# Kernel optimization log

Measured on AMD Instinct MI355X. Metric: run time of the kernel, lower is better.

The kernel has to match this reference:

```python
import jax, jax.numpy as jnp
import numpy as np

C = 64
G = 4
K = 3
GC = C // G
OS = 1.0  # offset_scale
OM_DIM = int(np.ceil(G * K * K * 3 / 8) * 8)  # 112, padded; only first G*27 used


def setup_inputs() -> dict:
    key = jax.random.key(0)
    ks = jax.random.split(key, 8)
    B, H, W = 2, 384, 384
    s = 0.02
    return {
        "inp": jax.random.normal(ks[0], (B, C, H, W), jnp.float32),
        "Wv": jax.random.normal(ks[1], (C, C), jnp.float32) * s,
        "bv": jnp.zeros((C,), jnp.float32),
        "Wdw": jax.random.normal(ks[2], (C, 1, K, K), jnp.float32) * s,
        "bdw": jnp.zeros((C,), jnp.float32),
        "Wom": jax.random.normal(ks[3], (C, OM_DIM), jnp.float32) * s,
        "bom": jnp.zeros((OM_DIM,), jnp.float32),
        "Wo": jax.random.normal(ks[4], (C, C), jnp.float32) * s,
    }


def _bilinear(v, px, py, H, W, b_idx, g_idx):
    # v: (B,H,W,G,GC); px,py: (B,H,W,G) pixel coords; zero padding outside.
    x0 = jnp.floor(px)
    y0 = jnp.floor(py)
    wx1 = px - x0
    wy1 = py - y0
    x0i = x0.astype(jnp.int32)
    y0i = y0.astype(jnp.int32)
    out = jnp.zeros(px.shape + (v.shape[-1],), v.dtype)
    for dy, wy in ((0, 1.0 - wy1), (1, wy1)):
        for dx, wx in ((0, 1.0 - wx1), (1, wx1)):
            xi = x0i + dx
            yi = y0i + dy
            valid = ((xi >= 0) & (xi < W) & (yi >= 0) & (yi < H)).astype(v.dtype)
            xc = jnp.clip(xi, 0, W - 1)
            yc = jnp.clip(yi, 0, H - 1)
            g = v[b_idx, yc, xc, g_idx]  # (B,H,W,G,GC)
            out = out + g * (wy * wx * valid)[..., None]
    return out


def reference(inp, Wv, bv, Wdw, bdw, Wom, bom, Wo):
    B, _, H, W = inp.shape
    x = inp.transpose(0, 2, 3, 1)  # (B,H,W,C)
    # value projection, split into groups
    value = (x @ Wv + bv).reshape(B, H, W, G, GC)
    # depthwise conv on input feeds the offset/mask predictor
    dw = jax.lax.conv_general_dilated(
        inp, Wdw, window_strides=(1, 1), padding=[(1, 1), (1, 1)],
        feature_group_count=C) + bdw[None, :, None, None]
    om = dw.transpose(0, 2, 3, 1) @ Wom + bom  # (B,H,W,OM_DIM)
    om = om[..., : G * K * K * 3].reshape(B, H, W, G, K * K * 3)
    off = om[..., : K * K * 2].reshape(B, H, W, G, K * K, 2)  # (dx,dy) per point
    mask = om[..., K * K * 2:]  # (B,H,W,G,K*K), no softmax in DCNv4

    base_x = jnp.arange(W, dtype=value.dtype)[None, None, :, None]
    base_y = jnp.arange(H, dtype=value.dtype)[None, :, None, None]
    b_idx = jnp.arange(B)[:, None, None, None]
    g_idx = jnp.arange(G)[None, None, None, :]

    out = jnp.zeros((B, H, W, G, GC), value.dtype)
    k = 0
    for ky in range(K):
        for kx in range(K):
            dx = off[..., k, 0]
            dy = off[..., k, 1]
            px = base_x + ((kx - K // 2) + dx) * OS
            py = base_y + ((ky - K // 2) + dy) * OS
            samp = _bilinear(value, px, py, H, W, b_idx, g_idx)
            out = out + samp * mask[..., k][..., None]
            k += 1

    out = out.reshape(B, H, W, C) @ Wo  # output_proj, no bias (output_bias=False)
    return out.transpose(0, 3, 1, 2)  # back to (B,C,H,W)
```

## Files before the change

kernel.cpp:

```cpp
#include <hip/hip_runtime.h>
#include <hip/hip_fp16.h>
#include <math.h>

namespace {
constexpr int kH = 384, kW = 384, kBn = 2;
constexpr int kHW = kH * kW;
constexpr int kOMD = 112;
constexpr int kNB = kBn * (kHW / 64);
constexpr int kNB8 = kNB / 8;
}

typedef _Float16 h2 __attribute__((ext_vector_type(2)));
typedef _Float16 half8 __attribute__((ext_vector_type(8)));
typedef float f32x4 __attribute__((ext_vector_type(4)));

__device__ unsigned g_Wom2[32 * kOMD];
__device__ unsigned g_Wo2[32 * 64];
__device__ __align__(16) _Float16 g_WvFh[4 * 2 * 64 * 8];
__device__ __align__(16) _Float16 g_WvFl[4 * 2 * 64 * 8];

__device__ __forceinline__ int swz(int t) {
    return (t & 7) * kNB8 + (t >> 3);
}

__device__ __forceinline__ unsigned pack2h(float a, float b) {
    unsigned short lo = __builtin_bit_cast(unsigned short, __float2half_rn(a));
    unsigned short hi = __builtin_bit_cast(unsigned short, __float2half_rn(b));
    return (unsigned)lo | ((unsigned)hi << 16);
}

#if __has_builtin(__builtin_amdgcn_fdot2)
__device__ __forceinline__ float dot2(unsigned a, unsigned b, float c) {
    return __builtin_amdgcn_fdot2(__builtin_bit_cast(h2, a),
                                  __builtin_bit_cast(h2, b), c, false);
}
#else
__device__ __forceinline__ float dot2(unsigned a, unsigned b, float c) {
    h2 ha = __builtin_bit_cast(h2, a), hb = __builtin_bit_cast(h2, b);
    c = fmaf((float)ha.x, (float)hb.x, c);
    c = fmaf((float)ha.y, (float)hb.y, c);
    return c;
}
#endif

__device__ __forceinline__ void acc8h(__half2* pa, const unsigned short* src,
                                      float wgt) {
    const uint4 u0 = ((const uint4*)src)[0];
    const uint4 u1 = ((const uint4*)src)[1];
    const __half2 w2 = __half2half2(__float2half_rn(wgt));
    pa[0] = __hfma2(w2, __builtin_bit_cast(__half2, u0.x), pa[0]);
    pa[1] = __hfma2(w2, __builtin_bit_cast(__half2, u0.y), pa[1]);
    pa[2] = __hfma2(w2, __builtin_bit_cast(__half2, u0.z), pa[2]);
    pa[3] = __hfma2(w2, __builtin_bit_cast(__half2, u0.w), pa[3]);
    pa[4] = __hfma2(w2, __builtin_bit_cast(__half2, u1.x), pa[4]);
    pa[5] = __hfma2(w2, __builtin_bit_cast(__half2, u1.y), pa[5]);
    pa[6] = __hfma2(w2, __builtin_bit_cast(__half2, u1.z), pa[6]);
    pa[7] = __hfma2(w2, __builtin_bit_cast(__half2, u1.w), pa[7]);
}

__device__ __forceinline__ half8 ld_frag_g(const _Float16* ptr) {
    return __builtin_bit_cast(half8, *(const uint4*)ptr);
}

__global__ __launch_bounds__(256) void k_prep(
        const float* __restrict__ Wv, const float* __restrict__ Wom,
        const float* __restrict__ Wo) {
    const int gt = blockIdx.x * 256 + threadIdx.x;
    const int gstep = 64 * 256;
    for (int i = gt; i < 4 * 2 * 64 * 8; i += gstep) {
        const int jj = i & 7, l = (i >> 3) & 63, kh = (i >> 9) & 1, mt = i >> 10;
        const int co = mt * 16 + (l & 15);
        const int ch = kh * 32 + ((l >> 4) & 3) * 8 + jj;
        const float w = Wv[ch * 64 + co];
        const _Float16 hi = (_Float16)w;
        g_WvFh[i] = hi;
        g_WvFl[i] = (_Float16)((w - (float)hi) * 2048.f);
    }
    for (int i = gt; i < 32 * kOMD; i += gstep) {
        const int ci2 = i / kOMD, j = i % kOMD;
        g_Wom2[i] = pack2h(Wom[(2 * ci2) * kOMD + j],
                           Wom[(2 * ci2 + 1) * kOMD + j]);
    }
    for (int i = gt; i < 32 * 64; i += gstep) {
        const int ci2 = i >> 6, j = i & 63;
        g_Wo2[i] = pack2h(Wo[(2 * ci2) * 64 + j],
                          Wo[(2 * ci2 + 1) * 64 + j]);
    }
}

__global__ __launch_bounds__(256) void k_value(
        const float* __restrict__ inp, const float* __restrict__ bv,
        unsigned short* __restrict__ value) {
    const int tid = threadIdx.x;
    const int bid = swz(blockIdx.x);
    const int b = bid / (kHW / 64);
    const int pix0 = (bid % (kHW / 64)) * 64;
    const int l = tid & 63;
    const int wv = tid >> 6;
    const int lr = l & 15, q = l >> 4;
    const int gpx = pix0 + wv * 16 + lr;

    const float* xb = inp + (size_t)b * 64 * kHW + (size_t)(q * 8) * kHW + gpx;
    half8 bhf[2], blf[2];
    #pragma unroll
    for (int kh = 0; kh < 2; ++kh) {
        float xv[8];
        #pragma unroll
        for (int jj = 0; jj < 8; ++jj)
            xv[jj] = xb[(size_t)(kh * 32 + jj) * kHW];
        half8 hh, ll;
        #pragma unroll
        for (int jj = 0; jj < 8; ++jj) {
            const _Float16 hval = (_Float16)xv[jj];
            hh[jj] = hval;
            ll[jj] = (_Float16)((xv[jj] - (float)hval) * 2048.f);
        }
        bhf[kh] = hh;
        blf[kh] = ll;
    }

    #pragma unroll
    for (int mt = 0; mt < 4; ++mt) {
        const half8 ah0 = ld_frag_g(g_WvFh + ((mt * 2 + 0) * 64 + l) * 8);
        const half8 ah1 = ld_frag_g(g_WvFh + ((mt * 2 + 1) * 64 + l) * 8);
        const half8 al0 = ld_frag_g(g_WvFl + ((mt * 2 + 0) * 64 + l) * 8);
        const half8 al1 = ld_frag_g(g_WvFl + ((mt * 2 + 1) * 64 + l) * 8);
        f32x4 acc = {0.f, 0.f, 0.f, 0.f};
        f32x4 acc2 = {0.f, 0.f, 0.f, 0.f};
        acc  = __builtin_amdgcn_mfma_f32_16x16x32_f16(ah0, bhf[0], acc, 0, 0, 0);
        acc  = __builtin_amdgcn_mfma_f32_16x16x32_f16(ah1, bhf[1], acc, 0, 0, 0);
        acc2 = __builtin_amdgcn_mfma_f32_16x16x32_f16(ah0, blf[0], acc2, 0, 0, 0);
        acc2 = __builtin_amdgcn_mfma_f32_16x16x32_f16(ah1, blf[1], acc2, 0, 0, 0);
        acc2 = __builtin_amdgcn_mfma_f32_16x16x32_f16(al0, bhf[0], acc2, 0, 0, 0);
        acc2 = __builtin_amdgcn_mfma_f32_16x16x32_f16(al1, bhf[1], acc2, 0, 0, 0);
        const float4 b4 = *(const float4*)(bv + mt * 16 + q * 4);
        const float v0 = acc[0] + acc2[0] * (1.f / 2048.f) + b4.x;
        const float v1 = acc[1] + acc2[1] * (1.f / 2048.f) + b4.y;
        const float v2 = acc[2] + acc2[2] * (1.f / 2048.f) + b4.z;
        const float v3 = acc[3] + acc2[3] * (1.f / 2048.f) + b4.w;
        uint2 st;
        st.x = pack2h(v0, v1);
        st.y = pack2h(v2, v3);
        *(uint2*)(value + ((size_t)(b * 4 + mt) * kHW + gpx) * 16 + q * 4) = st;
    }
}

__global__ __launch_bounds__(256) void k_main(
        const float* __restrict__ inp, const float* __restrict__ Wdw,
        const float* __restrict__ bdw, const float* __restrict__ bom,
        const unsigned short* __restrict__ value, float* __restrict__ out) {
    __shared__ unsigned lds2[32][64];

    const int tid = threadIdx.x;
    const int bid = swz(blockIdx.x);
    const int b = bid / (kH * (kW / 64));
    const int rem = bid % (kH * (kW / 64));
    const int h = rem / (kW / 64);
    const int w0 = (rem % (kW / 64)) * 64;

    const int p = tid & 63;
    const int gs = __builtin_amdgcn_readfirstlane(tid >> 6);

    if (w0 != 0 && w0 != kW - 64) {
        const int i2 = p & 31;
        const int ch8 = p >> 5;
        const int xg = w0 + 2 * i2;
        float s0[8], s1[8];
        #pragma unroll 4
        for (int cc = 0; cc < 8; ++cc) {
            const int cA = gs * 16 + cc;
            const int cB = cA + 8;
            const float bsv = ch8 ? bdw[cB] : bdw[cA];
            float a0 = bsv, a1 = bsv;
            const float* ibA = inp + (size_t)(b * 64 + cA) * kHW;
            const float* wkA = Wdw + cA * 9;
            const float* wkB = Wdw + cB * 9;
            #pragma unroll
            for (int r = 0; r < 3; ++r) {
                const int y = h - 1 + r;
                if (y >= 0 && y < kH) {
                    const float* rowp = ibA + (size_t)(ch8 * 8) * kHW
                                            + (size_t)y * kW;
                    const float2 fc = *(const float2*)(rowp + xg);
                    const float xl = rowp[xg - 1];
                    const float xr = rowp[xg + 2];
                    const float k0 = ch8 ? wkB[r * 3 + 0] : wkA[r * 3 + 0];
                    const float k1 = ch8 ? wkB[r * 3 + 1] : wkA[r * 3 + 1];
                    const float k2 = ch8 ? wkB[r * 3 + 2] : wkA[r * 3 + 2];
                    a0 = fmaf(xl,   k0, a0);
                    a0 = fmaf(fc.x, k1, a0);
                    a0 = fmaf(fc.y, k2, a0);
                    a1 = fmaf(fc.x, k0, a1);
                    a1 = fmaf(fc.y, k1, a1);
                    a1 = fmaf(xr,   k2, a1);
                }
            }
            s0[cc] = a0;
            s1[cc] = a1;
        }
        #pragma unroll
        for (int e = 0; e < 4; ++e) {
            const int row = gs * 8 + ch8 * 4 + e;
            lds2[row][2 * i2]     = pack2h(s0[2 * e], s0[2 * e + 1]);
            lds2[row][2 * i2 + 1] = pack2h(s1[2 * e], s1[2 * e + 1]);
        }
    } else {
        const int w = w0 + p;
        #pragma unroll 2
        for (int q = 0; q < 8; ++q) {
            float sv[2];
            #pragma unroll
            for (int e = 0; e < 2; ++e) {
                const int c = gs * 16 + 2 * q + e;
                const float* ib = inp + (size_t)(b * 64 + c) * kHW;
                float s = bdw[c];
                #pragma unroll
                for (int r = 0; r < 3; ++r) {
                    const int y = h - 1 + r;
                    if (y >= 0 && y < kH) {
                        const float* rowp = ib + (size_t)y * kW;
                        #pragma unroll
                        for (int kx = 0; kx < 3; ++kx) {
                            const int x = w - 1 + kx;
                            const float v = (x >= 0 && x < kW) ? rowp[x] : 0.f;
                            s = fmaf(v, Wdw[c * 9 + r * 3 + kx], s);
                        }
                    }
                }
                sv[e] = s;
            }
            lds2[gs * 8 + q][p] = pack2h(sv[0], sv[1]);
        }
    }
    __syncthreads();

    float om[27];
    {
        const float* bg = bom + gs * 27;
        #pragma unroll
        for (int j = 0; j < 27; ++j) om[j] = bg[j];
        #pragma unroll 4
        for (int ci2 = 0; ci2 < 32; ++ci2) {
            const unsigned a2 = lds2[ci2][p];
            const unsigned* wr = g_Wom2 + ci2 * kOMD + gs * 27;
            #pragma unroll
            for (int j = 0; j < 27; ++j) om[j] = dot2(a2, wr[j], om[j]);
        }
    }
    __syncthreads();

    {
        __half2 pa[8];
        #pragma unroll
        for (int j = 0; j < 8; ++j) pa[j] = __builtin_bit_cast(__half2, 0u);
        const float fw = (float)(w0 + p);
        const float fh = (float)h;
        const unsigned short* vbase = value + (size_t)(b * 4 + gs) * kHW * 16;
        #pragma unroll
        for (int k = 0; k < 9; ++k) {
            const int ky = k / 3, kx = k % 3;
            const float dx = om[2 * k];
            const float dy = om[2 * k + 1];
            const float m = om[18 + k];
            const float px = fw + (float)(kx - 1) + dx;
            const float py = fh + (float)(ky - 1) + dy;
            const float x0f = floorf(px), y0f = floorf(py);
            const int x0 = (int)x0f, y0 = (int)y0f;
            const float wx1 = px - x0f, wy1 = py - y0f;
            const float wx0 = 1.f - wx1, wy0 = 1.f - wy1;
            const bool interior = (x0 >= 0) & (y0 >= 0) &
                                  (x0 < kW - 1) & (y0 < kH - 1);
            if (__all(interior)) {
                const unsigned short* b00 = vbase + ((size_t)y0 * kW + x0) * 16;
                const float wy0m = wy0 * m, wy1m = wy1 * m;
                acc8h(pa, b00,                wx0 * wy0m);
                acc8h(pa, b00 + 16,           wx1 * wy0m);
                acc8h(pa, b00 + kW * 16,      wx0 * wy1m);
                acc8h(pa, b00 + kW * 16 + 16, wx1 * wy1m);
            } else {
                #pragma unroll
                for (int cor = 0; cor < 4; ++cor) {
                    const int dy2 = cor >> 1, dx2 = cor & 1;
                    const int xi = x0 + dx2, yi = y0 + dy2;
                    float wgt = (dy2 ? wy1 : wy0) * (dx2 ? wx1 : wx0) * m;
                    if (xi < 0 || xi >= kW || yi < 0 || yi >= kH) wgt = 0.f;
                    const int xc = min(max(xi, 0), kW - 1);
                    const int yc = min(max(yi, 0), kH - 1);
                    acc8h(pa, vbase + ((size_t)yc * kW + xc) * 16, wgt);
                }
            }
        }
        #pragma unroll
        for (int j = 0; j < 8; ++j)
            lds2[gs * 8 + j][p] = __builtin_bit_cast(unsigned, pa[j]);
    }
    __syncthreads();

    {
        float acc[16];
        #pragma unroll
        for (int j = 0; j < 16; ++j) acc[j] = 0.f;
        #pragma unroll 4
        for (int ci2 = 0; ci2 < 32; ++ci2) {
            const unsigned a2 = lds2[ci2][p];
            const unsigned* wr = g_Wo2 + ci2 * 64 + gs * 16;
            #pragma unroll
            for (int j = 0; j < 16; ++j) acc[j] = dot2(a2, wr[j], acc[j]);
        }
        float* ob = out + (size_t)(b * 64 + gs * 16) * kHW + (size_t)h * kW + w0 + p;
        #pragma unroll
        for (int j = 0; j < 16; ++j) ob[(size_t)j * kHW] = acc[j];
    }
}

extern "C" void kernel_launch(void* const* d_in, const int* in_sizes, int n_in,
                              void* d_out, int out_size, void* d_ws, size_t ws_size,
                              hipStream_t stream) {
    const float* inp = (const float*)d_in[0];
    const float* Wv  = (const float*)d_in[1];
    const float* bv  = (const float*)d_in[2];
    const float* Wdw = (const float*)d_in[3];
    const float* bdw = (const float*)d_in[4];
    const float* Wom = (const float*)d_in[5];
    const float* bom = (const float*)d_in[6];
    const float* Wo  = (const float*)d_in[7];
    float* outp = (float*)d_out;
    unsigned short* value = (unsigned short*)d_ws;

    k_prep<<<64, 256, 0, stream>>>(Wv, Wom, Wo);
    k_value<<<kNB, 256, 0, stream>>>(inp, bv, value);
    k_main<<<kNB, 256, 0, stream>>>(inp, Wdw, bdw, bom, value, outp);
}
```

Baseline: 299.1 us.

## Split offset/mask prediction into a kernel co-scheduled with value projection

Interleaves value-projection blocks with depthwise-conv plus offset/mask blocks in a single launch, writing the offsets and masks as fp16 to a workspace buffer. A separate kernel then reads them and does the deformable sampling and output projection. The aim is to overlap the conv/offset compute with the memory-bound value projection and to lighten the sampling kernel, at the cost of extra global traffic and fp16 rounding of offsets. The previous two-kernel path is kept as a fallback when the workspace is too small.

```diff
diff --git a/kernel.cpp b/kernel.cpp
--- a/kernel.cpp
+++ b/kernel.cpp
@@ -8,6 +8,8 @@
 constexpr int kOMD = 112;
 constexpr int kNB = kBn * (kHW / 64);
 constexpr int kNB8 = kNB / 8;
+constexpr size_t kValBytes = (size_t)kBn * 4 * kHW * 16 * 2;
+constexpr size_t kOmBytes  = (size_t)kBn * 4 * kHW * 32 * 2;
 }
 
 typedef _Float16 h2 __attribute__((ext_vector_type(2)));
@@ -27,6 +29,15 @@
     unsigned short lo = __builtin_bit_cast(unsigned short, __float2half_rn(a));
     unsigned short hi = __builtin_bit_cast(unsigned short, __float2half_rn(b));
     return (unsigned)lo | ((unsigned)hi << 16);
+}
+
+__device__ __forceinline__ float h2f_lo(unsigned u) {
+    __half2 h = __builtin_bit_cast(__half2, u);
+    return __half2float(h.x);
+}
+__device__ __forceinline__ float h2f_hi(unsigned u) {
+    __half2 h = __builtin_bit_cast(__half2, u);
+    return __half2float(h.y);
 }
 
 #if __has_builtin(__builtin_amdgcn_fdot2)
@@ -62,43 +73,16 @@
     return __builtin_bit_cast(half8, *(const uint4*)ptr);
 }
 
-__global__ __launch_bounds__(256) void k_prep(
-        const float* __restrict__ Wv, const float* __restrict__ Wom,
-        const float* __restrict__ Wo) {
-    const int gt = blockIdx.x * 256 + threadIdx.x;
-    const int gstep = 64 * 256;
-    for (int i = gt; i < 4 * 2 * 64 * 8; i += gstep) {
-        const int jj = i & 7, l = (i >> 3) & 63, kh = (i >> 9) & 1, mt = i >> 10;
-        const int co = mt * 16 + (l & 15);
-        const int ch = kh * 32 + ((l >> 4) & 3) * 8 + jj;
-        const float w = Wv[ch * 64 + co];
-        const _Float16 hi = (_Float16)w;
-        g_WvFh[i] = hi;
-        g_WvFl[i] = (_Float16)((w - (float)hi) * 2048.f);
-    }
-    for (int i = gt; i < 32 * kOMD; i += gstep) {
-        const int ci2 = i / kOMD, j = i % kOMD;
-        g_Wom2[i] = pack2h(Wom[(2 * ci2) * kOMD + j],
-                           Wom[(2 * ci2 + 1) * kOMD + j]);
-    }
-    for (int i = gt; i < 32 * 64; i += gstep) {
-        const int ci2 = i >> 6, j = i & 63;
-        g_Wo2[i] = pack2h(Wo[(2 * ci2) * 64 + j],
-                          Wo[(2 * ci2 + 1) * 64 + j]);
-    }
-}
-
-__global__ __launch_bounds__(256) void k_value(
+
+__device__ __forceinline__ void value_body(
         const float* __restrict__ inp, const float* __restrict__ bv,
-        unsigned short* __restrict__ value) {
-    const int tid = threadIdx.x;
-    const int bid = swz(blockIdx.x);
+        unsigned short* __restrict__ value, int t, int tid) {
+    const int bid = swz(t);
     const int b = bid / (kHW / 64);
     const int pix0 = (bid % (kHW / 64)) * 64;
     const int l = tid & 63;
-    const int wv = tid >> 6;
-    const int lr = l & 15, q = l >> 4;
-    const int gpx = pix0 + wv * 16 + lr;
+    const int q = l >> 4;
+    const int gpx = pix0 + (tid >> 6) * 16 + (l & 15);
 
     const float* xb = inp + (size_t)b * 64 * kHW + (size_t)(q * 8) * kHW + gpx;
     half8 bhf[2], blf[2];
@@ -118,7 +102,6 @@
         bhf[kh] = hh;
         blf[kh] = ll;
     }
-
     #pragma unroll
     for (int mt = 0; mt < 4; ++mt) {
         const half8 ah0 = ld_frag_g(g_WvFh + ((mt * 2 + 0) * 64 + l) * 8);
@@ -134,33 +117,19 @@
         acc2 = __builtin_amdgcn_mfma_f32_16x16x32_f16(al0, bhf[0], acc2, 0, 0, 0);
         acc2 = __builtin_amdgcn_mfma_f32_16x16x32_f16(al1, bhf[1], acc2, 0, 0, 0);
         const float4 b4 = *(const float4*)(bv + mt * 16 + q * 4);
-        const float v0 = acc[0] + acc2[0] * (1.f / 2048.f) + b4.x;
-        const float v1 = acc[1] + acc2[1] * (1.f / 2048.f) + b4.y;
-        const float v2 = acc[2] + acc2[2] * (1.f / 2048.f) + b4.z;
-        const float v3 = acc[3] + acc2[3] * (1.f / 2048.f) + b4.w;
         uint2 st;
-        st.x = pack2h(v0, v1);
-        st.y = pack2h(v2, v3);
+        st.x = pack2h(acc[0] + acc2[0] * (1.f / 2048.f) + b4.x,
+                      acc[1] + acc2[1] * (1.f / 2048.f) + b4.y);
+        st.y = pack2h(acc[2] + acc2[2] * (1.f / 2048.f) + b4.z,
+                      acc[3] + acc2[3] * (1.f / 2048.f) + b4.w);
         *(uint2*)(value + ((size_t)(b * 4 + mt) * kHW + gpx) * 16 + q * 4) = st;
     }
 }
 
-__global__ __launch_bounds__(256) void k_main(
+__device__ __forceinline__ void stageA_conv(
         const float* __restrict__ inp, const float* __restrict__ Wdw,
-        const float* __restrict__ bdw, const float* __restrict__ bom,
-        const unsigned short* __restrict__ value, float* __restrict__ out) {
-    __shared__ unsigned lds2[32][64];
-
-    const int tid = threadIdx.x;
-    const int bid = swz(blockIdx.x);
-    const int b = bid / (kH * (kW / 64));
-    const int rem = bid % (kH * (kW / 64));
-    const int h = rem / (kW / 64);
-    const int w0 = (rem % (kW / 64)) * 64;
-
-    const int p = tid & 63;
-    const int gs = __builtin_amdgcn_readfirstlane(tid >> 6);
-
+        const float* __restrict__ bdw, int b, int h, int w0, int p, int gs,
+        unsigned (*lds2)[64]) {
     if (w0 != 0 && w0 != kW - 64) {
         const int i2 = p & 31;
         const int ch8 = p >> 5;
@@ -232,23 +201,27 @@
             lds2[gs * 8 + q][p] = pack2h(sv[0], sv[1]);
         }
     }
-    __syncthreads();
-
-    float om[27];
-    {
-        const float* bg = bom + gs * 27;
-        #pragma unroll
-        for (int j = 0; j < 27; ++j) om[j] = bg[j];
-        #pragma unroll 4
-        for (int ci2 = 0; ci2 < 32; ++ci2) {
-            const unsigned a2 = lds2[ci2][p];
-            const unsigned* wr = g_Wom2 + ci2 * kOMD + gs * 27;
-            #pragma unroll
-            for (int j = 0; j < 27; ++j) om[j] = dot2(a2, wr[j], om[j]);
-        }
-    }
-    __syncthreads();
-
+}
+
+__device__ __forceinline__ void stageB_om(
+        const float* __restrict__ bom, int p, int gs,
+        const unsigned (*lds2)[64], float* om) {
+    const float* bg = bom + gs * 27;
+    #pragma unroll
+    for (int j = 0; j < 27; ++j) om[j] = bg[j];
+    #pragma unroll 4
+    for (int ci2 = 0; ci2 < 32; ++ci2) {
+        const unsigned a2 = lds2[ci2][p];
+        const unsigned* wr = g_Wom2 + ci2 * kOMD + gs * 27;
+        #pragma unroll
+        for (int j = 0; j < 27; ++j) om[j] = dot2(a2, wr[j], om[j]);
+    }
+}
+
+__device__ __forceinline__ void stageCD(
+        const float* om, const unsigned short* __restrict__ value,
+        float* __restrict__ out, int b, int h, int w0, int p, int gs,
+        unsigned (*lds2)[64]) {
     {
         __half2 pa[8];
         #pragma unroll
@@ -295,7 +268,6 @@
             lds2[gs * 8 + j][p] = __builtin_bit_cast(unsigned, pa[j]);
     }
     __syncthreads();
-
     {
         float acc[16];
         #pragma unroll
@@ -311,6 +283,125 @@
         #pragma unroll
         for (int j = 0; j < 16; ++j) ob[(size_t)j * kHW] = acc[j];
     }
+}
+
+
+__global__ __launch_bounds__(256) void k_prep(
+        const float* __restrict__ Wv, const float* __restrict__ Wom,
+        const float* __restrict__ Wo) {
+    const int gt = blockIdx.x * 256 + threadIdx.x;
+    const int gstep = 64 * 256;
+    for (int i = gt; i < 4 * 2 * 64 * 8; i += gstep) {
+        const int jj = i & 7, l = (i >> 3) & 63, kh = (i >> 9) & 1, mt = i >> 10;
+        const int co = mt * 16 + (l & 15);
+        const int ch = kh * 32 + ((l >> 4) & 3) * 8 + jj;
+        const float w = Wv[ch * 64 + co];
+        const _Float16 hi = (_Float16)w;
+        g_WvFh[i] = hi;
+        g_WvFl[i] = (_Float16)((w - (float)hi) * 2048.f);
+    }
+    for (int i = gt; i < 32 * kOMD; i += gstep) {
+        const int ci2 = i / kOMD, j = i % kOMD;
+        g_Wom2[i] = pack2h(Wom[(2 * ci2) * kOMD + j],
+                           Wom[(2 * ci2 + 1) * kOMD + j]);
+    }
+    for (int i = gt; i < 32 * 64; i += gstep) {
+        const int ci2 = i >> 6, j = i & 63;
+        g_Wo2[i] = pack2h(Wo[(2 * ci2) * 64 + j],
+                          Wo[(2 * ci2 + 1) * 64 + j]);
+    }
+}
+
+__global__ __launch_bounds__(256) void k_fuse1(
+        const float* __restrict__ inp, const float* __restrict__ bv,
+        const float* __restrict__ Wdw, const float* __restrict__ bdw,
+        const float* __restrict__ bom, unsigned short* __restrict__ value,
+        unsigned short* __restrict__ omws) {
+    __shared__ unsigned lds2[32][64];
+    const int tid = threadIdx.x;
+    const int t = blockIdx.x >> 1;
+    if ((blockIdx.x & 1) == 0) {
+        value_body(inp, bv, value, t, tid);
+        return;
+    }
+    const int bid = swz(t);
+    const int b = bid / (kH * (kW / 64));
+    const int rem = bid % (kH * (kW / 64));
+    const int h = rem / (kW / 64);
+    const int w0 = (rem % (kW / 64)) * 64;
+    const int p = tid & 63;
+    const int gs = __builtin_amdgcn_readfirstlane(tid >> 6);
+
+    stageA_conv(inp, Wdw, bdw, b, h, w0, p, gs, lds2);
+    __syncthreads();
+    float om[27];
+    stageB_om(bom, p, gs, lds2, om);
+    unsigned short* obase = omws +
+            ((size_t)(b * 4 + gs) * kHW + (size_t)h * kW + w0 + p) * 32;
+    *(uint4*)obase = make_uint4(pack2h(om[0], om[1]),  pack2h(om[2], om[3]),
+                                pack2h(om[4], om[5]),  pack2h(om[6], om[7]));
+    *(uint4*)(obase + 8) = make_uint4(pack2h(om[8], om[9]),   pack2h(om[10], om[11]),
+                                      pack2h(om[12], om[13]), pack2h(om[14], om[15]));
+    *(uint4*)(obase + 16) = make_uint4(pack2h(om[16], om[17]), pack2h(om[18], om[19]),
+                                       pack2h(om[20], om[21]), pack2h(om[22], om[23]));
+    *(uint2*)(obase + 24) = make_uint2(pack2h(om[24], om[25]), pack2h(om[26], 0.f));
+}
+
+__global__ __launch_bounds__(256) void k_pv(
+        const unsigned short* __restrict__ omws,
+        const unsigned short* __restrict__ value, float* __restrict__ out) {
+    __shared__ unsigned lds2[32][64];
+    const int tid = threadIdx.x;
+    const int bid = swz(blockIdx.x);
+    const int b = bid / (kH * (kW / 64));
+    const int rem = bid % (kH * (kW / 64));
+    const int h = rem / (kW / 64);
+    const int w0 = (rem % (kW / 64)) * 64;
+    const int p = tid & 63;
+    const int gs = __builtin_amdgcn_readfirstlane(tid >> 6);
+
+    const unsigned short* obase = omws +
+            ((size_t)(b * 4 + gs) * kHW + (size_t)h * kW + w0 + p) * 32;
+    const uint4 r0 = *(const uint4*)obase;
+    const uint4 r1 = *(const uint4*)(obase + 8);
+    const uint4 r2 = *(const uint4*)(obase + 16);
+    const uint2 r3 = *(const uint2*)(obase + 24);
+    const unsigned rr[14] = {r0.x, r0.y, r0.z, r0.w, r1.x, r1.y, r1.z, r1.w,
+                             r2.x, r2.y, r2.z, r2.w, r3.x, r3.y};
+    float om[27];
+    #pragma unroll
+    for (int j = 0; j < 27; ++j)
+        om[j] = (j & 1) ? h2f_hi(rr[j >> 1]) : h2f_lo(rr[j >> 1]);
+
+    stageCD(om, value, out, b, h, w0, p, gs, lds2);
+}
+
+__global__ __launch_bounds__(256) void k_value_fb(
+        const float* __restrict__ inp, const float* __restrict__ bv,
+        unsigned short* __restrict__ value) {
+    value_body(inp, bv, value, blockIdx.x, threadIdx.x);
+}
+
+__global__ __launch_bounds__(256) void k_main_fb(
+        const float* __restrict__ inp, const float* __restrict__ Wdw,
+        const float* __restrict__ bdw, const float* __restrict__ bom,
+        const unsigned short* __restrict__ value, float* __restrict__ out) {
+    __shared__ unsigned lds2[32][64];
+    const int tid = threadIdx.x;
+    const int bid = swz(blockIdx.x);
+    const int b = bid / (kH * (kW / 64));
+    const int rem = bid % (kH * (kW / 64));
+    const int h = rem / (kW / 64);
+    const int w0 = (rem % (kW / 64)) * 64;
+    const int p = tid & 63;
+    const int gs = __builtin_amdgcn_readfirstlane(tid >> 6);
+
+    stageA_conv(inp, Wdw, bdw, b, h, w0, p, gs, lds2);
+    __syncthreads();
+    float om[27];
+    stageB_om(bom, p, gs, lds2, om);
+    __syncthreads();
+    stageCD(om, value, out, b, h, w0, p, gs, lds2);
 }
 
 extern "C" void kernel_launch(void* const* d_in, const int* in_sizes, int n_in,
@@ -328,6 +419,12 @@
     unsigned short* value = (unsigned short*)d_ws;
 
     k_prep<<<64, 256, 0, stream>>>(Wv, Wom, Wo);
-    k_value<<<kNB, 256, 0, stream>>>(inp, bv, value);
-    k_main<<<kNB, 256, 0, stream>>>(inp, Wdw, bdw, bom, value, outp);
-}
+    if (ws_size >= kValBytes + kOmBytes) {
+        unsigned short* omws = (unsigned short*)((char*)d_ws + kValBytes);
+        k_fuse1<<<2 * kNB, 256, 0, stream>>>(inp, bv, Wdw, bdw, bom, value, omws);
+        k_pv<<<kNB, 256, 0, stream>>>(omws, value, outp);
+    } else {
+        k_value_fb<<<kNB, 256, 0, stream>>>(inp, bv, value);
+        k_main_fb<<<kNB, 256, 0, stream>>>(inp, Wdw, bdw, bom, value, outp);
+    }
+}
```

Result: slower. 359.2 us (+20.1%).

## Switch main kernel tiles from 1x64 rows to 16x4 2D pixel tiles

Applied to the files above, without the earlier changes.

Each block now covers a 16-wide by 4-tall pixel patch instead of a 64-pixel row segment, and the specialised interior depthwise path is replaced by the generic per-pixel stencil for all blocks. The 2D tile is meant to improve cache locality for the bilinear gathers from the value tensor, since sampled neighbours span rows, and for the 3x3 depthwise stencil. The trade-off is that global loads and output stores become 16-float row segments rather than 64-float ones, so coalescing is weaker, and the vectorised float2 interior conv path is gone.

```diff
diff --git a/kernel.cpp b/kernel.cpp
--- a/kernel.cpp
+++ b/kernel.cpp
@@ -8,6 +8,8 @@
 constexpr int kOMD = 112;
 constexpr int kNB = kBn * (kHW / 64);
 constexpr int kNB8 = kNB / 8;
+constexpr int kTX = kW / 16;
+constexpr int kTY = kH / 4;
 }
 
 typedef _Float16 h2 __attribute__((ext_vector_type(2)));
@@ -153,65 +155,26 @@
 
     const int tid = threadIdx.x;
     const int bid = swz(blockIdx.x);
-    const int b = bid / (kH * (kW / 64));
-    const int rem = bid % (kH * (kW / 64));
-    const int h = rem / (kW / 64);
-    const int w0 = (rem % (kW / 64)) * 64;
+    const int b = bid / (kTX * kTY);
+    const int rem = bid % (kTX * kTY);
+    const int ty = rem / kTX;
+    const int tx = rem % kTX;
+    const int h0 = ty * 4;
+    const int w0 = tx * 16;
 
     const int p = tid & 63;
+    const int dx16 = p & 15, dy4 = p >> 4;
+    const int w = w0 + dx16;
+    const int h = h0 + dy4;
     const int gs = __builtin_amdgcn_readfirstlane(tid >> 6);
 
-    if (w0 != 0 && w0 != kW - 64) {
-        const int i2 = p & 31;
-        const int ch8 = p >> 5;
-        const int xg = w0 + 2 * i2;
-        float s0[8], s1[8];
-        #pragma unroll 4
-        for (int cc = 0; cc < 8; ++cc) {
-            const int cA = gs * 16 + cc;
-            const int cB = cA + 8;
-            const float bsv = ch8 ? bdw[cB] : bdw[cA];
-            float a0 = bsv, a1 = bsv;
-            const float* ibA = inp + (size_t)(b * 64 + cA) * kHW;
-            const float* wkA = Wdw + cA * 9;
-            const float* wkB = Wdw + cB * 9;
-            #pragma unroll
-            for (int r = 0; r < 3; ++r) {
-                const int y = h - 1 + r;
-                if (y >= 0 && y < kH) {
-                    const float* rowp = ibA + (size_t)(ch8 * 8) * kHW
-                                            + (size_t)y * kW;
-                    const float2 fc = *(const float2*)(rowp + xg);
-                    const float xl = rowp[xg - 1];
-                    const float xr = rowp[xg + 2];
-                    const float k0 = ch8 ? wkB[r * 3 + 0] : wkA[r * 3 + 0];
-                    const float k1 = ch8 ? wkB[r * 3 + 1] : wkA[r * 3 + 1];
-                    const float k2 = ch8 ? wkB[r * 3 + 2] : wkA[r * 3 + 2];
-                    a0 = fmaf(xl,   k0, a0);
-                    a0 = fmaf(fc.x, k1, a0);
-                    a0 = fmaf(fc.y, k2, a0);
-                    a1 = fmaf(fc.x, k0, a1);
-                    a1 = fmaf(fc.y, k1, a1);
-                    a1 = fmaf(xr,   k2, a1);
-                }
-            }
-            s0[cc] = a0;
-            s1[cc] = a1;
-        }
-        #pragma unroll
-        for (int e = 0; e < 4; ++e) {
-            const int row = gs * 8 + ch8 * 4 + e;
-            lds2[row][2 * i2]     = pack2h(s0[2 * e], s0[2 * e + 1]);
-            lds2[row][2 * i2 + 1] = pack2h(s1[2 * e], s1[2 * e + 1]);
-        }
-    } else {
-        const int w = w0 + p;
+    {
         #pragma unroll 2
-        for (int q = 0; q < 8; ++q) {
+        for (int cq = 0; cq < 8; ++cq) {
             float sv[2];
             #pragma unroll
             for (int e = 0; e < 2; ++e) {
-                const int c = gs * 16 + 2 * q + e;
+                const int c = gs * 16 + 2 * cq + e;
                 const float* ib = inp + (size_t)(b * 64 + c) * kHW;
                 float s = bdw[c];
                 #pragma unroll
@@ -229,7 +192,7 @@
                 }
                 sv[e] = s;
             }
-            lds2[gs * 8 + q][p] = pack2h(sv[0], sv[1]);
+            lds2[gs * 8 + cq][p] = pack2h(sv[0], sv[1]);
         }
     }
     __syncthreads();
@@ -253,17 +216,17 @@
         __half2 pa[8];
         #pragma unroll
         for (int j = 0; j < 8; ++j) pa[j] = __builtin_bit_cast(__half2, 0u);
-        const float fw = (float)(w0 + p);
+        const float fw = (float)w;
         const float fh = (float)h;
         const unsigned short* vbase = value + (size_t)(b * 4 + gs) * kHW * 16;
         #pragma unroll
         for (int k = 0; k < 9; ++k) {
             const int ky = k / 3, kx = k % 3;
-            const float dx = om[2 * k];
-            const float dy = om[2 * k + 1];
+            const float dxo = om[2 * k];
+            const float dyo = om[2 * k + 1];
             const float m = om[18 + k];
-            const float px = fw + (float)(kx - 1) + dx;
-            const float py = fh + (float)(ky - 1) + dy;
+            const float px = fw + (float)(kx - 1) + dxo;
+            const float py = fh + (float)(ky - 1) + dyo;
             const float x0f = floorf(px), y0f = floorf(py);
             const int x0 = (int)x0f, y0 = (int)y0f;
             const float wx1 = px - x0f, wy1 = py - y0f;
@@ -307,7 +270,7 @@
             #pragma unroll
             for (int j = 0; j < 16; ++j) acc[j] = dot2(a2, wr[j], acc[j]);
         }
-        float* ob = out + (size_t)(b * 64 + gs * 16) * kHW + (size_t)h * kW + w0 + p;
+        float* ob = out + (size_t)(b * 64 + gs * 16) * kHW + (size_t)h * kW + w;
         #pragma unroll
         for (int j = 0; j < 16; ++j) ob[(size_t)j * kHW] = acc[j];
     }
```

After: 300.4 us. About the same (+0.4%).
